# Optimization experiments

Measured on AMD Instinct MI355X. Metric: run time of the kernel, lower is better.

Reference implementation:

```python
import jax, jax.numpy as jnp
import numpy as np

N = 10000      # nodes
IN_DIM = 512   # input feature dim
HID = 512      # GCN hidden dim
OUT = 256      # embedding dim
E = 320000     # edges (avg degree 32)


def _normalize(x, eps=1e-12):
    # F.normalize: x / max(||x||_2, eps), row-wise
    n = jnp.sqrt(jnp.sum(x * x, axis=-1, keepdims=True))
    return x / jnp.maximum(n, eps)


def _gcn_conv(x, W, b, src, dst, n):
    # DGL GraphConv with norm='both': D_out^{-1/2} -> sum-aggregate -> D_in^{-1/2}, then bias
    ones = jnp.ones(src.shape[0], x.dtype)
    deg_out = jax.ops.segment_sum(ones, src, num_segments=n)
    deg_in = jax.ops.segment_sum(ones, dst, num_segments=n)
    ns = jnp.where(deg_out > 0, deg_out ** -0.5, 0.0)
    nd = jnp.where(deg_in > 0, deg_in ** -0.5, 0.0)
    h = x @ W                                  # weight first (math-equivalent)
    msg = h[src] * ns[src, None]               # gather + src-normalize
    agg = jax.ops.segment_sum(msg, dst, num_segments=n)  # scatter-sum to dst
    return agg * nd[:, None] + b


def _gcn(x, params, src, dst, n):
    W0, b0, W1, b1 = params
    h = jax.nn.relu(_gcn_conv(x, W0, b0, src, dst, n))
    return _gcn_conv(h, W1, b1, src, dst, n)


def _scores(v, u, Wp, bp, src, dst, n, tau):
    # pos_score: edge sim = <normalize(u)[src], normalize(proj(v))[dst]> / tau, scatter-mean to dst
    q = _normalize(v @ Wp + bp)
    un = _normalize(u)
    sim = jnp.sum(un[src] * q[dst], axis=1) / tau          # [E]
    cnt = jax.ops.segment_sum(jnp.ones_like(sim), dst, num_segments=n)
    denom = jnp.maximum(cnt, 1.0)                          # DGL mean gives 0 for deg-0 nodes
    pos = jax.ops.segment_sum(sim, dst, num_segments=n) / denom
    # neg_score: per-node total similarity (intra + inter), then per-edge log, scatter-mean
    z = _normalize(v)
    stu = _normalize(u)
    neg_sim = jnp.exp(z @ z.T / tau).sum(1) + jnp.exp(z @ stu.T / tau).sum(1)  # [N]
    m = jnp.log(neg_sim[dst] + jnp.exp(sim))               # udf_u_add_log_e
    neg = jax.ops.segment_sum(m, dst, num_segments=n) / denom
    return pos, neg


def setup_inputs() -> dict:
    key = jax.random.key(0)
    ks = jax.random.split(key, 16)
    feat = jax.random.normal(ks[0], (N, IN_DIM), jnp.float32)
    src_g = jax.random.randint(ks[1], (E,), 0, N)
    dst_g = jax.random.randint(ks[2], (E,), 0, N)
    src_s = jax.random.randint(ks[3], (E,), 0, N)
    dst_s = jax.random.randint(ks[4], (E,), 0, N)

    def lin(k, i, o, s=0.05):
        return jax.random.normal(k, (i, o), jnp.float32) * s

    inp = dict(
        feat=feat, src_g=src_g, dst_g=dst_g, src_s=src_s, dst_s=dst_s,
        tau1=jnp.ones((), jnp.float32), tau2=jnp.ones((), jnp.float32),
        # encoder1 (GCN, 2 layers) online + target (deepcopy -> independent params)
        W1a=lin(ks[5], IN_DIM, HID), b1a=jnp.zeros((HID,), jnp.float32),
        W1b=lin(ks[6], HID, OUT), b1b=jnp.zeros((OUT,), jnp.float32),
        W1a_t=lin(ks[7], IN_DIM, HID), b1a_t=jnp.zeros((HID,), jnp.float32),
        W1b_t=lin(ks[8], HID, OUT), b1b_t=jnp.zeros((OUT,), jnp.float32),
        # encoder2 (Linear) online + target
        W2=lin(ks[9], IN_DIM, OUT), b2=jnp.zeros((OUT,), jnp.float32),
        W2_t=lin(ks[10], IN_DIM, OUT), b2_t=jnp.zeros((OUT,), jnp.float32),
        # projector: Predictor(out, out, num_layers=1) -> single Linear
        Wp=lin(ks[11], OUT, OUT), bp=jnp.zeros((OUT,), jnp.float32),
    )
    return inp


def reference(feat, src_g, dst_g, src_s, dst_s, tau1, tau2,
              W1a, b1a, W1b, b1b, W1a_t, b1a_t, W1b_t, b1b_t,
              W2, b2, W2_t, b2_t, Wp, bp):
    n = feat.shape[0]
    # branch 1: GCN encoder
    v1 = _gcn(feat, (W1a, b1a, W1b, b1b), src_g, dst_g, n)
    u1 = _gcn(feat, (W1a_t, b1a_t, W1b_t, b1b_t), src_g, dst_g, n)
    pos1, neg1 = _scores(v1, u1, Wp, bp, src_s, dst_s, n, tau1)
    loss1 = jnp.mean(-pos1 + neg1)
    # branch 2: linear encoder
    v2 = feat @ W2 + b2
    u2 = feat @ W2_t + b2_t
    pos2, neg2 = _scores(v2, u2, Wp, bp, src_s, dst_s, n, tau2)
    loss2 = jnp.mean(-pos2 + neg2)
    return (v1, u1, v2, u2, loss1 + loss2)
```

## Files before the change

### kernel.cpp

```cpp
#include <hip/hip_runtime.h>

typedef __bf16 bf16x8 __attribute__((ext_vector_type(8)));
typedef float f32x4 __attribute__((ext_vector_type(4)));
typedef unsigned short u16x8 __attribute__((ext_vector_type(8)));

#define GLOAD16(gp, lp) __builtin_amdgcn_global_load_lds( \
    (const __attribute__((address_space(1))) void*)(gp), \
    (__attribute__((address_space(3))) void*)(lp), 16, 0, 0)

__device__ __forceinline__ unsigned short f2bf(float f) {
  union { float f; unsigned u; } c; c.f = f;
  unsigned u = c.u;
  u = (u + 0x7fffu + ((u >> 16) & 1u)) >> 16;
  return (unsigned short)u;
}
__device__ __forceinline__ float b2f(unsigned short u) {
  union { unsigned u; float f; } c; c.u = ((unsigned)u) << 16; return c.f;
}

__global__ void k_count(const int* __restrict__ src_g, const int* __restrict__ dst_g,
                        const int* __restrict__ dst_s,
                        int* deg_og, int* deg_ig, int* cnt_s, int E)
{
  int e = blockIdx.x * blockDim.x + threadIdx.x;
  if (e >= E) return;
  atomicAdd(&deg_og[src_g[e]], 1);
  atomicAdd(&deg_ig[dst_g[e]], 1);
  atomicAdd(&cnt_s[dst_s[e]], 1);
}

__global__ void k_norms(const int* __restrict__ deg_og, const int* __restrict__ deg_ig,
                        float* __restrict__ ns, float* __restrict__ nd, int N)
{
  int i = blockIdx.x * blockDim.x + threadIdx.x;
  if (i >= N) return;
  int a = deg_og[i]; ns[i] = a > 0 ? rsqrtf((float)a) : 0.f;
  int b = deg_ig[i]; nd[i] = b > 0 ? rsqrtf((float)b) : 0.f;
}

__global__ __launch_bounds__(1024) void k_scan(const int* __restrict__ deg0, int* __restrict__ offs0,
                                               const int* __restrict__ deg1, int* __restrict__ offs1, int N)
{
  const int* deg = blockIdx.x ? deg1 : deg0;
  int* offs = blockIdx.x ? offs1 : offs0;
  __shared__ int lds[1024];
  __shared__ int carry_s;
  const int t = threadIdx.x;
  if (t == 0) { carry_s = 0; offs[0] = 0; }
  __syncthreads();
  for (int base = 0; base < N; base += 1024) {
    const int i = base + t;
    int v = (i < N) ? deg[i] : 0;
    lds[t] = v;
    __syncthreads();
    for (int o = 1; o < 1024; o <<= 1) {
      int tmp = (t >= o) ? lds[t - o] : 0;
      __syncthreads();
      lds[t] += tmp;
      __syncthreads();
    }
    const int carry = carry_s;
    if (i < N) offs[i + 1] = lds[t] + carry;
    __syncthreads();
    if (t == 1023) carry_s = carry + lds[1023];
    __syncthreads();
  }
}

__global__ void k_fill(const int* __restrict__ srcA, const int* __restrict__ dstA,
                       const int* __restrict__ offsA, int* curA, int* __restrict__ outA,
                       const int* __restrict__ srcB, const int* __restrict__ dstB,
                       const int* __restrict__ offsB, int* curB, int* __restrict__ outB, int E)
{
  int e = blockIdx.x * blockDim.x + threadIdx.x;
  if (e >= E) return;
  if (blockIdx.y == 0) {
    int d = dstA[e];
    int p = atomicAdd(&curA[d], 1);
    outA[offsA[d] + p] = srcA[e];
  } else {
    int d = dstB[e];
    int p = atomicAdd(&curB[d], 1);
    outB[offsB[d] + p] = srcB[e];
  }
}

struct PrepArgs {
  const float *feat, *W1a, *W1at, *W1b, *W1bt, *W2, *W2t, *Wp;
  const float *b1a, *b1at, *b1b, *b1bt, *b2, *b2t;
  unsigned short *featb, *wcatL1, *wcat2, *wcatLin, *wtp;
  float *bcatL1, *bcatGcn, *bcatLin;
  int NF;
};
__global__ void k_prep(PrepArgs p)
{
  int i = blockIdx.x * blockDim.x + threadIdx.x;
  if (i < p.NF) { p.featb[i] = f2bf(p.feat[i]); return; }
  i -= p.NF;
  if (i < 1024 * 512) {
    int n = i >> 9, k = i & 511;
    p.wcatL1[i] = f2bf(n < 512 ? p.W1a[k * 512 + n] : p.W1at[k * 512 + n - 512]);
    return;
  }
  i -= 1024 * 512;
  if (i < 512 * 512) {
    int n = i >> 9, k = i & 511;
    p.wcat2[i] = f2bf(n < 256 ? p.W1b[k * 256 + n] : p.W1bt[k * 256 + n - 256]);
    return;
  }
  i -= 512 * 512;
  if (i < 512 * 512) {
    int n = i >> 9, k = i & 511;
    p.wcatLin[i] = f2bf(n < 256 ? p.W2[k * 256 + n] : p.W2t[k * 256 + n - 256]);
    return;
  }
  i -= 512 * 512;
  if (i < 256 * 256) {
    int n = i >> 8, k = i & 255;
    p.wtp[i] = f2bf(p.Wp[k * 256 + n]);
    return;
  }
  i -= 256 * 256;
  if (i < 1024) { p.bcatL1[i] = i < 512 ? p.b1a[i] : p.b1at[i - 512]; return; }
  i -= 1024;
  if (i < 512) { p.bcatGcn[i] = i < 256 ? p.b1b[i] : p.b1bt[i - 256]; return; }
  i -= 512;
  if (i < 512) { p.bcatLin[i] = i < 256 ? p.b2[i] : p.b2t[i - 256]; return; }
}

__global__ __launch_bounds__(256) void k_mgemm(
    const unsigned short* __restrict__ A, int lda,
    const unsigned short* __restrict__ Wt,
    const float* __restrict__ bias, float* __restrict__ outf, unsigned short* __restrict__ outb,
    int M, int K, int Nc, int relu, int asel, int splitM)
{
  __shared__ char smem[24576];
  char* As = smem;
  char* Bs = smem + 16384;
  const int tid = threadIdx.x;
  const int lane = tid & 63, w = tid >> 6;
  const int wr = w >> 1, wc = w & 1;
  const int bm = blockIdx.x * 128, bn = blockIdx.y * 64;
  const int aoff = (asel > 0 && bn >= asel) ? K : 0;
  const int srow = lane >> 3;
  const int scol = ((lane & 7) ^ srow) << 3;
  const int xr = (lane & 7) << 4;

  f32x4 acc[4][2];
  #pragma unroll
  for (int mi = 0; mi < 4; ++mi)
    #pragma unroll
    for (int nj = 0; nj < 2; ++nj)
      acc[mi][nj] = (f32x4){0.f, 0.f, 0.f, 0.f};

  for (int k0 = 0; k0 < K; k0 += 64) {
    #pragma unroll
    for (int i = 0; i < 4; ++i) {
      int row = w * 32 + i * 8 + srow;
      int rg = bm + row; rg = rg < M ? rg : M - 1;
      GLOAD16(A + (size_t)rg * lda + aoff + k0 + scol, As + (w * 4096 + i * 1024));
    }
    #pragma unroll
    for (int i = 0; i < 2; ++i) {
      int nrow = w * 16 + i * 8 + srow;
      GLOAD16(Wt + (size_t)(bn + nrow) * K + k0 + scol, Bs + (w * 2048 + i * 1024));
    }
    __syncthreads();
    #pragma unroll
    for (int ks = 0; ks < 2; ++ks) {
      const int kb = ks * 64 + ((lane >> 4) << 4);
      bf16x8 af[4], bfr[2];
      #pragma unroll
      for (int mi = 0; mi < 4; ++mi) {
        int row_l = wr * 64 + mi * 16 + (lane & 15);
        af[mi] = *(const bf16x8*)(As + row_l * 128 + (kb ^ xr));
      }
      #pragma unroll
      for (int nj = 0; nj < 2; ++nj) {
        int n_l = wc * 32 + nj * 16 + (lane & 15);
        bfr[nj] = *(const bf16x8*)(Bs + n_l * 128 + (kb ^ xr));
      }
      __builtin_amdgcn_s_setprio(1);
      #pragma unroll
      for (int mi = 0; mi < 4; ++mi)
        #pragma unroll
        for (int nj = 0; nj < 2; ++nj)
          acc[mi][nj] = __builtin_amdgcn_mfma_f32_16x16x32_bf16(af[mi], bfr[nj], acc[mi][nj], 0, 0, 0);
      __builtin_amdgcn_s_setprio(0);
    }
    __syncthreads();
  }

  #pragma unroll
  for (int mi = 0; mi < 4; ++mi) {
    #pragma unroll
    for (int j = 0; j < 4; ++j) {
      int r = bm + wr * 64 + mi * 16 + ((lane >> 4) << 2) + j;
      if (r >= M) continue;
      #pragma unroll
      for (int nj = 0; nj < 2; ++nj) {
        int c = bn + wc * 32 + nj * 16 + (lane & 15);
        float v = acc[mi][nj][j];
        if (bias) v += bias[c];
        if (relu) v = fmaxf(v, 0.f);
        if (splitM > 0) {
          int rr = r + (c >= 256 ? splitM : 0);
          if (outf) outf[(size_t)rr * 256 + (c & 255)] = v;
          if (outb && c < 256) outb[(size_t)r * 256 + c] = f2bf(v);
        } else {
          if (outf) outf[(size_t)r * Nc + c] = v;
          if (outb) outb[(size_t)r * Nc + c] = f2bf(v);
        }
      }
    }
  }
}

__global__ __launch_bounds__(256) void k_agg(const unsigned short* __restrict__ h,
    const int* __restrict__ offs, const int* __restrict__ csr,
    const float* __restrict__ ns, const float* __restrict__ nd, const float* __restrict__ bias,
    float* __restrict__ outf, unsigned short* __restrict__ outb, int relu, int splitM)
{
  const int node = blockIdx.x * 4 + (threadIdx.x >> 6);
  const int lane = threadIdx.x & 63;
  const int j = lane * 8;
  const int s0 = offs[node], s1 = offs[node + 1];
  float a[8] = {};
  for (int k = s0; k < s1; ++k) {
    const int s = csr[k];
    const float w = ns[s];
    const u16x8 hv = *(const u16x8*)(h + (size_t)s * 512 + j);
    #pragma unroll
    for (int q = 0; q < 8; ++q) a[q] += b2f(hv[q]) * w;
  }
  const float ndv = nd[node];
  float o[8];
  #pragma unroll
  for (int q = 0; q < 8; ++q) {
    o[q] = a[q] * ndv;
    if (bias) o[q] += bias[j + q];
    if (relu) o[q] = fmaxf(o[q], 0.f);
  }
  if (splitM > 0) {
    const int rr = node + (j >= 256 ? splitM : 0);
    const int cc = j & 255;
    if (outf) {
      *(float4*)(outf + (size_t)rr * 256 + cc)     = (float4){o[0], o[1], o[2], o[3]};
      *(float4*)(outf + (size_t)rr * 256 + cc + 4) = (float4){o[4], o[5], o[6], o[7]};
    }
    if (outb && j < 256) {
      u16x8 ub;
      #pragma unroll
      for (int q = 0; q < 8; ++q) ub[q] = f2bf(o[q]);
      *(u16x8*)(outb + (size_t)node * 256 + j) = ub;
    }
  } else {
    if (outf) {
      *(float4*)(outf + (size_t)node * 512 + j)     = (float4){o[0], o[1], o[2], o[3]};
      *(float4*)(outf + (size_t)node * 512 + j + 4) = (float4){o[4], o[5], o[6], o[7]};
    }
    if (outb) {
      u16x8 ub;
      #pragma unroll
      for (int q = 0; q < 8; ++q) ub[q] = f2bf(o[q]);
      *(u16x8*)(outb + (size_t)node * 512 + j) = ub;
    }
  }
}

__global__ __launch_bounds__(256) void k_normrows3(
    const float* __restrict__ X0, unsigned short* __restrict__ O0,
    const float* __restrict__ X1, unsigned short* __restrict__ O1,
    const float* __restrict__ X2, unsigned short* __restrict__ O2, int Nrows)
{
  const float* X = blockIdx.y == 0 ? X0 : (blockIdx.y == 1 ? X1 : X2);
  unsigned short* O = blockIdx.y == 0 ? O0 : (blockIdx.y == 1 ? O1 : O2);
  const int wid = threadIdx.x >> 6, lane = threadIdx.x & 63;
  const int row = blockIdx.x * 4 + wid;
  if (row >= Nrows) return;
  const float4 v = ((const float4*)(X + (size_t)row * 256))[lane];
  float ss = v.x * v.x + v.y * v.y + v.z * v.z + v.w * v.w;
  #pragma unroll
  for (int m = 1; m < 64; m <<= 1) ss += __shfl_xor(ss, m);
  const float inv = 1.f / fmaxf(sqrtf(ss), 1e-12f);
  ushort4 u;
  u.x = f2bf(v.x * inv); u.y = f2bf(v.y * inv);
  u.z = f2bf(v.z * inv); u.w = f2bf(v.w * inv);
  ((ushort4*)(O + (size_t)row * 256))[lane] = u;
}

__global__ __launch_bounds__(256) void k_edge(
    const unsigned short* __restrict__ zun1, const unsigned short* __restrict__ zun2,
    const unsigned short* __restrict__ qb,
    const int* __restrict__ offs_s, const int* __restrict__ csr_es,
    const float* __restrict__ tau1p, const float* __restrict__ tau2p,
    const float* __restrict__ negs1, const float* __restrict__ negs2,
    float* __restrict__ pos1, float* __restrict__ neg1,
    float* __restrict__ pos2, float* __restrict__ neg2, int N)
{
  const int node = blockIdx.x * 4 + (threadIdx.x >> 6);
  if (node >= N) return;
  const int z = blockIdx.y;
  const unsigned short* un = (z ? zun2 : zun1) + (size_t)N * 256;
  const unsigned short* q = qb + (size_t)z * N * 256;
  const float inv_tau = 1.f / (z ? tau2p[0] : tau1p[0]);
  const float nsd = (z ? negs2 : negs1)[node];
  float* pos = z ? pos2 : pos1;
  float* neg = z ? neg2 : neg1;
  const int lane = threadIdx.x & 63;
  const int l = lane & 31, h = lane >> 5;
  const u16x8 qv = *(const u16x8*)(q + (size_t)node * 256 + l * 8);
  float qf[8];
  #pragma unroll
  for (int i = 0; i < 8; ++i) qf[i] = b2f(qv[i]);
  const int s0 = offs_s[node], s1 = offs_s[node + 1];
  float pacc = 0.f, nacc = 0.f;
  for (int k = s0 + h; k < s1; k += 2) {
    const int s = csr_es[k];
    const u16x8 av = *(const u16x8*)(un + (size_t)s * 256 + l * 8);
    float dot = 0.f;
    #pragma unroll
    for (int i = 0; i < 8; ++i) dot += b2f(av[i]) * qf[i];
    #pragma unroll
    for (int m = 1; m < 32; m <<= 1) dot += __shfl_xor(dot, m);
    if (l == 0) {
      const float sv = dot * inv_tau;
      pacc += sv;
      nacc += logf(nsd + __expf(sv));
    }
  }
  pacc += __shfl_xor(pacc, 32);
  nacc += __shfl_xor(nacc, 32);
  if (lane == 0) { pos[node] = pacc; neg[node] = nacc; }
}

#define NEG_JSPLIT 16
#define NEG_TILES 4
__global__ __launch_bounds__(256) void k_negsim(
    const unsigned short* __restrict__ zun1, const unsigned short* __restrict__ zun2,
    const float* __restrict__ tau1p, const float* __restrict__ tau2p,
    float* __restrict__ negs1, float* __restrict__ negs2, int N)
{
  __shared__ char smem[32768];
  const int tid = threadIdx.x;
  const int lane = tid & 63, wid = tid >> 6;
  const int z = blockIdx.z;
  const unsigned short* zun = z ? zun2 : zun1;
  float* negsim = z ? negs2 : negs1;
  const float k_exp = 1.0f / (z ? tau2p[0] : tau1p[0]);
  const int ntiles = N >> 4;
  int itv[NEG_TILES]; bool vv[NEG_TILES];
  #pragma unroll
  for (int t = 0; t < NEG_TILES; ++t) {
    int it = blockIdx.x * (4 * NEG_TILES) + wid * NEG_TILES + t;
    vv[t] = it < ntiles;
    itv[t] = vv[t] ? it : (ntiles - 1);
  }

  bf16x8 afrag[NEG_TILES][8];
  #pragma unroll
  for (int t = 0; t < NEG_TILES; ++t) {
    const unsigned short* r = zun + (size_t)((itv[t] << 4) + (lane & 15)) * 256 + ((lane >> 4) << 3);
    #pragma unroll
    for (int ks = 0; ks < 8; ++ks)
      afrag[t][ks] = *(const bf16x8*)(r + ks * 32);
  }

  const int total = 2 * N;
  const int chunk = ((total + NEG_JSPLIT * 32 - 1) / (NEG_JSPLIT * 32)) * 32;
  const int jbeg = blockIdx.y * chunk;
  const int jend = min(total, jbeg + chunk);
  if (jbeg >= jend) return;

  float psum[NEG_TILES][4];
  #pragma unroll
  for (int t = 0; t < NEG_TILES; ++t)
    #pragma unroll
    for (int j = 0; j < 4; ++j) psum[t][j] = 0.f;

  auto stage = [&](int buf, int j0) {
    #pragma unroll
    for (int i = 0; i < 4; ++i) {
      int idx = tid + 256 * i;
      int r = idx >> 5, c = idx & 31;
      int g = j0 + r; g = g < total ? g : total - 1;
      int cp = c ^ (r & 7);
      GLOAD16(zun + (size_t)g * 256 + cp * 8, smem + buf * 16384 + r * 512 + c * 16);
    }
  };

  const int rxor = (lane & 7) << 4;
  const int kcol = (lane >> 4) << 4;
  int cur = 0;
  stage(0, jbeg);
  __syncthreads();
  for (int j0 = jbeg; j0 < jend; j0 += 32) {
    if (j0 + 32 < jend) stage(cur ^ 1, j0 + 32);
    const int rows = min(32, jend - j0);
    const int nsub = rows >> 4;
    const char* base = smem + cur * 16384;
    for (int sub = 0; sub < nsub; ++sub) {
      const char* bb = base + (sub * 16 + (lane & 15)) * 512;
      f32x4 acc[NEG_TILES];
      #pragma unroll
      for (int t = 0; t < NEG_TILES; ++t) acc[t] = (f32x4){0.f, 0.f, 0.f, 0.f};
      __builtin_amdgcn_s_setprio(1);
      #pragma unroll
      for (int ks = 0; ks < 8; ++ks) {
        bf16x8 bfrag = *(const bf16x8*)(bb + ((kcol + ks * 64) ^ rxor));
        #pragma unroll
        for (int t = 0; t < NEG_TILES; ++t)
          acc[t] = __builtin_amdgcn_mfma_f32_16x16x32_bf16(afrag[t][ks], bfrag, acc[t], 0, 0, 0);
      }
      __builtin_amdgcn_s_setprio(0);
      #pragma unroll
      for (int t = 0; t < NEG_TILES; ++t)
        #pragma unroll
        for (int j = 0; j < 4; ++j)
          psum[t][j] += __expf(acc[t][j] * k_exp);
    }
    __syncthreads();
    cur ^= 1;
  }
  #pragma unroll
  for (int t = 0; t < NEG_TILES; ++t)
    #pragma unroll
    for (int j = 0; j < 4; ++j) {
      float x = psum[t][j];
      x += __shfl_xor(x, 1);
      x += __shfl_xor(x, 2);
      x += __shfl_xor(x, 4);
      x += __shfl_xor(x, 8);
      if (vv[t] && (lane & 15) == 0)
        atomicAdd(&negsim[(itv[t] << 4) + ((lane >> 4) << 2) + j], x);
    }
}

__global__ __launch_bounds__(1024) void k_loss(
    const float* __restrict__ pos1, const float* __restrict__ neg1,
    const float* __restrict__ pos2, const float* __restrict__ neg2,
    const int* __restrict__ cnt, int N, float* __restrict__ out)
{
  __shared__ float lds[1024];
  float s = 0.f;
  for (int i = threadIdx.x; i < N; i += 1024) {
    float denom = fmaxf((float)cnt[i], 1.f);
    s += ((-pos1[i] + neg1[i]) + (-pos2[i] + neg2[i])) / denom;
  }
  lds[threadIdx.x] = s;
  __syncthreads();
  for (int o = 512; o > 0; o >>= 1) {
    if (threadIdx.x < o) lds[threadIdx.x] += lds[threadIdx.x + o];
    __syncthreads();
  }
  if (threadIdx.x == 0) out[0] = lds[0] / (float)N;
}

extern "C" void kernel_launch(void* const* d_in, const int* in_sizes, int n_in,
                              void* d_out, int out_size, void* d_ws, size_t ws_size,
                              hipStream_t stream)
{
  const float* feat  = (const float*)d_in[0];
  const int* src_g   = (const int*)d_in[1];
  const int* dst_g   = (const int*)d_in[2];
  const int* src_s   = (const int*)d_in[3];
  const int* dst_s   = (const int*)d_in[4];
  const float* tau1  = (const float*)d_in[5];
  const float* tau2  = (const float*)d_in[6];
  const float* W1a   = (const float*)d_in[7];
  const float* b1a   = (const float*)d_in[8];
  const float* W1b   = (const float*)d_in[9];
  const float* b1b   = (const float*)d_in[10];
  const float* W1a_t = (const float*)d_in[11];
  const float* b1a_t = (const float*)d_in[12];
  const float* W1b_t = (const float*)d_in[13];
  const float* b1b_t = (const float*)d_in[14];
  const float* W2    = (const float*)d_in[15];
  const float* b2    = (const float*)d_in[16];
  const float* W2_t  = (const float*)d_in[17];
  const float* b2_t  = (const float*)d_in[18];
  const float* Wp    = (const float*)d_in[19];
  const float* bp    = (const float*)d_in[20];

  const int N = in_sizes[0] / 512;
  const int E = in_sizes[1];

  float* out  = (float*)d_out;
  float* v1u1 = out;
  float* v2u2 = out + (size_t)2 * N * 256;
  float* loss = out + (size_t)4 * N * 256;

  char* ws = (char*)d_ws;
  size_t off = 0;
  auto alloc = [&](size_t bytes) -> char* {
    char* p = ws + off;
    off += (bytes + 255) & ~(size_t)255;
    return p;
  };
  int* zbase    = (int*)alloc((size_t)11 * N * 4);
  int* deg_og   = zbase;
  int* deg_ig   = zbase + N;
  int* cnt_s    = zbase + 2 * N;
  int* cursor   = zbase + 3 * N;
  int* cursor_s = zbase + 4 * N;
  float* pos1   = (float*)(zbase + 5 * N);
  float* neg1   = (float*)(zbase + 6 * N);
  float* pos2   = (float*)(zbase + 7 * N);
  float* neg2   = (float*)(zbase + 8 * N);
  float* negs1  = (float*)(zbase + 9 * N);
  float* negs2  = (float*)(zbase + 10 * N);
  int* offs    = (int*)alloc((size_t)(N + 1) * 4);
  int* offs_s  = (int*)alloc((size_t)(N + 1) * 4);
  int* csr_src = (int*)alloc((size_t)E * 4);
  int* csr_es  = (int*)alloc((size_t)E * 4);
  float* ns    = (float*)alloc((size_t)N * 4);
  float* nd    = (float*)alloc((size_t)N * 4);
  unsigned short* featb   = (unsigned short*)alloc((size_t)N * 512 * 2);
  unsigned short* wcatL1  = (unsigned short*)alloc((size_t)1024 * 512 * 2);
  unsigned short* wcat2   = (unsigned short*)alloc((size_t)512 * 512 * 2);
  unsigned short* wcatLin = (unsigned short*)alloc((size_t)512 * 512 * 2);
  unsigned short* wtp     = (unsigned short*)alloc((size_t)256 * 256 * 2);
  float* bcatL1  = (float*)alloc(1024 * 4);
  float* bcatGcn = (float*)alloc(512 * 4);
  float* bcatLin = (float*)alloc(512 * 4);
  char* BUF_H = alloc((size_t)N * 2048);
  char* BUF_A = alloc((size_t)N * 1024);
  char* BUF_B = alloc((size_t)N * 1024);
  char* BUF_C = alloc((size_t)N * 1024);
  char* BUF_E = alloc((size_t)N * 1024);
  if (off > ws_size) return;

  unsigned short* Xaggb = (unsigned short*)BUF_A;
  unsigned short* hcat  = (unsigned short*)BUF_H;
  unsigned short* g2cat = (unsigned short*)BUF_A;
  unsigned short* v1b   = (unsigned short*)BUF_E;
  float*          q_raw = (float*)BUF_H;
  unsigned short* qb    = (unsigned short*)BUF_A;
  unsigned short* zun1  = (unsigned short*)BUF_B;
  unsigned short* zun2  = (unsigned short*)BUF_C;

  const int eb = (E + 255) / 256;
  const int gmx = (N + 127) / 128;
  const int gqx = (2 * N + 127) / 128;
  const int ntiles = N / 16;
  const int ngroups = (ntiles + 4 * NEG_TILES - 1) / (4 * NEG_TILES);
  const dim3 neggrid(ngroups, NEG_JSPLIT, 2);
  const dim3 edgegrid((N + 3) / 4, 2);
  const dim3 nrmgrid((2 * N + 3) / 4, 3);

  hipMemsetAsync(zbase, 0, (size_t)11 * N * 4, stream);
  k_count<<<eb, 256, 0, stream>>>(src_g, dst_g, dst_s, deg_og, deg_ig, cnt_s, E);
  k_norms<<<(N + 255) / 256, 256, 0, stream>>>(deg_og, deg_ig, ns, nd, N);
  k_scan<<<2, 1024, 0, stream>>>(deg_ig, offs, cnt_s, offs_s, N);
  k_fill<<<dim3(eb, 2), 256, 0, stream>>>(src_g, dst_g, offs, cursor, csr_src,
                                          src_s, dst_s, offs_s, cursor_s, csr_es, E);

  PrepArgs pa;
  pa.feat = feat; pa.W1a = W1a; pa.W1at = W1a_t; pa.W1b = W1b; pa.W1bt = W1b_t;
  pa.W2 = W2; pa.W2t = W2_t; pa.Wp = Wp;
  pa.b1a = b1a; pa.b1at = b1a_t; pa.b1b = b1b; pa.b1bt = b1b_t; pa.b2 = b2; pa.b2t = b2_t;
  pa.featb = featb; pa.wcatL1 = wcatL1; pa.wcat2 = wcat2; pa.wcatLin = wcatLin; pa.wtp = wtp;
  pa.bcatL1 = bcatL1; pa.bcatGcn = bcatGcn; pa.bcatLin = bcatLin;
  pa.NF = N * 512;
  const int ptotal = pa.NF + 1024 * 512 + 512 * 512 + 512 * 512 + 256 * 256 + 1024 + 512 + 512;
  k_prep<<<(ptotal + 255) / 256, 256, 0, stream>>>(pa);

  k_agg<<<N / 4, 256, 0, stream>>>(featb, offs, csr_src, ns, nd, nullptr, nullptr, Xaggb, 0, 0);
  k_mgemm<<<dim3(gmx, 16), 256, 0, stream>>>(Xaggb, 512, wcatL1, bcatL1, nullptr, hcat,
                                             N, 512, 1024, 1, 0, 0);
  k_mgemm<<<dim3(gmx, 8), 256, 0, stream>>>(hcat, 1024, wcat2, nullptr, nullptr, g2cat,
                                            N, 512, 512, 0, 256, 0);
  k_agg<<<N / 4, 256, 0, stream>>>(g2cat, offs, csr_src, ns, nd, bcatGcn, v1u1, v1b, 0, N);
  k_mgemm<<<dim3(gmx, 8), 256, 0, stream>>>(featb, 512, wcatLin, bcatLin, v2u2,
                                            (unsigned short*)BUF_E + (size_t)N * 256,
                                            N, 512, 512, 0, 0, N);
  k_mgemm<<<dim3(gqx, 4), 256, 0, stream>>>((unsigned short*)BUF_E, 256, wtp, bp, q_raw, nullptr,
                                            2 * N, 256, 256, 0, 0, 0);

  k_normrows3<<<nrmgrid, 256, 0, stream>>>(v1u1, zun1, v2u2, zun2, q_raw, qb, 2 * N);

  k_negsim<<<neggrid, 256, 0, stream>>>(zun1, zun2, tau1, tau2, negs1, negs2, N);
  k_edge<<<edgegrid, 256, 0, stream>>>(zun1, zun2, qb, offs_s, csr_es, tau1, tau2,
                                       negs1, negs2, pos1, neg1, pos2, neg2, N);
  k_loss<<<1, 1024, 0, stream>>>(pos1, neg1, pos2, neg2, cnt_s, N, loss);
}
```

Baseline: 625.8 us.

## Prefetch neg-sim tiles two ahead with vmcnt waits; chunked single-pass scan

The negative-similarity kernel now issues global-to-LDS loads two tiles ahead. It uses explicit s_waitcnt vmcnt counts and raw s_barrier instead of full __syncthreads, so the next tile's loads stay in flight during MFMA compute. The degree prefix scan changes from repeated 1024-wide block scans with a carry to per-thread chunk sums, one block scan, and a local rewrite. This removes many barrier rounds. The hand-written waitcnt and barrier placement relies on exact load counts and ordering, which is fragile if the compiler reorders memory operations.

```diff
diff --git a/kernel.cpp b/kernel.cpp
--- a/kernel.cpp
+++ b/kernel.cpp
@@ -43,27 +43,28 @@
 {
   const int* deg = blockIdx.x ? deg1 : deg0;
   int* offs = blockIdx.x ? offs1 : offs0;
-  __shared__ int lds[1024];
-  __shared__ int carry_s;
+  __shared__ int part[1024];
   const int t = threadIdx.x;
-  if (t == 0) { carry_s = 0; offs[0] = 0; }
+  const int CH = (N + 1023) / 1024;
+  const int b = t * CH;
+  int s = 0;
+  for (int i = 0; i < CH; ++i) {
+    int idx = b + i;
+    s += (idx < N) ? deg[idx] : 0;
+  }
+  part[t] = s;
   __syncthreads();
-  for (int base = 0; base < N; base += 1024) {
-    const int i = base + t;
-    int v = (i < N) ? deg[i] : 0;
-    lds[t] = v;
+  for (int o = 1; o < 1024; o <<= 1) {
+    int v = (t >= o) ? part[t - o] : 0;
     __syncthreads();
-    for (int o = 1; o < 1024; o <<= 1) {
-      int tmp = (t >= o) ? lds[t - o] : 0;
-      __syncthreads();
-      lds[t] += tmp;
-      __syncthreads();
-    }
-    const int carry = carry_s;
-    if (i < N) offs[i + 1] = lds[t] + carry;
+    part[t] += v;
     __syncthreads();
-    if (t == 1023) carry_s = carry + lds[1023];
-    __syncthreads();
+  }
+  int run = (t == 0) ? 0 : part[t - 1];
+  if (t == 0) offs[0] = 0;
+  for (int i = 0; i < CH; ++i) {
+    int idx = b + i;
+    if (idx < N) { run += deg[idx]; offs[idx + 1] = run; }
   }
 }
 
@@ -393,9 +394,12 @@
   const int kcol = (lane >> 4) << 4;
   int cur = 0;
   stage(0, jbeg);
-  __syncthreads();
+  if (jbeg + 32 < jend) stage(1, jbeg + 32);
   for (int j0 = jbeg; j0 < jend; j0 += 32) {
-    if (j0 + 32 < jend) stage(cur ^ 1, j0 + 32);
+    if (j0 + 32 < jend) asm volatile("s_waitcnt vmcnt(4)" ::: "memory");
+    else                asm volatile("s_waitcnt vmcnt(0)" ::: "memory");
+    __builtin_amdgcn_sched_barrier(0);
+    asm volatile("s_barrier" ::: "memory");
     const int rows = min(32, jend - j0);
     const int nsub = rows >> 4;
     const char* base = smem + cur * 16384;
@@ -419,7 +423,8 @@
         for (int j = 0; j < 4; ++j)
           psum[t][j] += __expf(acc[t][j] * k_exp);
     }
-    __syncthreads();
+    asm volatile("s_barrier" ::: "memory");
+    if (j0 + 64 < jend) stage(cur, j0 + 64);
     cur ^= 1;
   }
   #pragma unroll
```

Result: slower. 639.0 us (+2.1%).
